# Kernel tuning notes

Measured on AMD Instinct MI355X. Metric: run time of the kernel, lower is better.

Reference implementation:

```python
import jax, jax.numpy as jnp
import numpy as np

N = 50000   # nodes
E = 300000  # edges
D = 256     # emb_dim
L = 5       # num_layers
BN_EPS = 1e-5


def setup_inputs() -> dict:
    key = jax.random.key(0)
    ks = jax.random.split(key, 6)
    scale = 0.05
    return {
        "x": jax.random.normal(ks[0], (N, D), jnp.float32),
        "src": jax.random.randint(ks[1], (E,), 0, N, dtype=jnp.int32),
        "dst": jax.random.randint(ks[2], (E,), 0, N, dtype=jnp.int32),
        "W1": jax.random.normal(ks[3], (L, D, D), jnp.float32) * scale,
        "b1": jnp.zeros((L, D), jnp.float32),
        "g1": jnp.ones((L, D), jnp.float32),
        "bt1": jnp.zeros((L, D), jnp.float32),
        "W2": jax.random.normal(ks[4], (L, D, D), jnp.float32) * scale,
        "b2": jnp.zeros((L, D), jnp.float32),
        "eps": jnp.zeros((L,), jnp.float32),
        "bn_g": jnp.ones((L, D), jnp.float32),
        "bn_b": jnp.zeros((L, D), jnp.float32),
    }


def _bn(h, gamma, beta):
    # torch BatchNorm1d training-mode forward: biased batch stats over nodes
    mean = jnp.mean(h, axis=0)
    var = jnp.var(h, axis=0)
    return (h - mean) * jax.lax.rsqrt(var + BN_EPS) * gamma + beta


def reference(x, src, dst, W1, b1, g1, bt1, W2, b2, eps, bn_g, bn_b):
    h = x
    for l in range(L):
        # GINConv: gather relu(x[src]) -> scatter-sum to dst
        msg = jax.nn.relu(h[src])                          # [E, D]
        agg = jax.ops.segment_sum(msg, dst, num_segments=N)  # [N, D]
        z = (1.0 + eps[l]) * h + agg
        # mlp: Linear -> BN -> ReLU -> Linear
        z = z @ W1[l] + b1[l]
        z = jax.nn.relu(_bn(z, g1[l], bt1[l]))
        z = z @ W2[l] + b2[l]
        # per-layer BatchNorm; dropout is identity (eval / drop_ratio=0)
        z = _bn(z, bn_g[l], bn_b[l])
        if l < L - 1:
            z = jax.nn.relu(z)
        h = z
    return h  # JK='last'
```

## Files before the change

kernel.cpp:

```cpp
#include <hip/hip_runtime.h>
#include <hip/hip_bf16.h>

#define N_NODES 50000
#define N_EDGES 300000
#define DIM 256
#define MPAD 50048

typedef __attribute__((ext_vector_type(8))) _Float16 half8;
typedef __attribute__((ext_vector_type(4))) _Float16 half4;
typedef __attribute__((ext_vector_type(4))) float f32x4;

__device__ __forceinline__ void async16(const void* g, void* l) {
    __builtin_amdgcn_global_load_lds(
        (const __attribute__((address_space(1))) unsigned int*)g,
        (__attribute__((address_space(3))) unsigned int*)l, 16, 0, 0);
}

__global__ __launch_bounds__(256) void hist_dst(const int* __restrict__ dst,
                                                int* __restrict__ deg, int E) {
    int e = blockIdx.x * blockDim.x + threadIdx.x;
    if (e < E) atomicAdd(&deg[dst[e]], 1);
}

__global__ __launch_bounds__(1024) void scan_blk(const int* __restrict__ deg,
                                                 int* __restrict__ ptr,
                                                 int* __restrict__ bsum, int n) {
    __shared__ int wsum[16];
    __shared__ int wpre[16];
    int tid = threadIdx.x;
    int i = blockIdx.x * 1024 + tid;
    int v = (i < n) ? deg[i] : 0;
    int lane = tid & 63, w = tid >> 6;
    int s = v;
#pragma unroll
    for (int off = 1; off < 64; off <<= 1) {
        int t = __shfl_up(s, off, 64);
        if (lane >= off) s += t;
    }
    if (lane == 63) wsum[w] = s;
    __syncthreads();
    if (tid < 16) {
        int acc = 0;
        for (int j = 0; j < tid; j++) acc += wsum[j];
        wpre[tid] = acc;
    }
    __syncthreads();
    int incl = s + wpre[w];
    if (i < n) ptr[i] = incl - v;
    if (tid == 1023) bsum[blockIdx.x] = incl;
}

__global__ __launch_bounds__(1024) void scan_add(int* __restrict__ ptr,
                                                 const int* __restrict__ bsum,
                                                 int* __restrict__ cursor,
                                                 int n, int E) {
    __shared__ int soff;
    int tid = threadIdx.x;
    if (tid < 64) {
        int v = (tid < (int)blockIdx.x) ? bsum[tid] : 0;
#pragma unroll
        for (int off = 32; off > 0; off >>= 1) v += __shfl_down(v, off, 64);
        if (tid == 0) soff = v;
    }
    __syncthreads();
    int i = blockIdx.x * 1024 + tid;
    if (i < n) {
        int val = ptr[i] + soff;
        ptr[i] = val;
        cursor[i] = val;
    }
    if (i == n) ptr[n] = E;
}

__global__ __launch_bounds__(256) void scatter_src(const int* __restrict__ src,
                                                   const int* __restrict__ dst,
                                                   int* __restrict__ cursor,
                                                   int* __restrict__ srcbuf, int E) {
    int e = blockIdx.x * blockDim.x + threadIdx.x;
    if (e < E) {
        int pos = atomicAdd(&cursor[dst[e]], 1);
        srcbuf[pos] = src[e];
    }
}

__global__ __launch_bounds__(256) void prep(const float* __restrict__ W1,
                                            const float* __restrict__ W2,
                                            _Float16* __restrict__ Wt,
                                            const float* __restrict__ x,
                                            _Float16* __restrict__ hb) {
    __shared__ float tile[64][65];
    int tid = threadIdx.x;
    if (blockIdx.x < 160) {
        int mat = blockIdx.x >> 4;
        int t = blockIdx.x & 15;
        int tr = t >> 2, tc = t & 3;
        const float* W = (mat < 5) ? (W1 + (size_t)mat * 65536)
                                   : (W2 + (size_t)(mat - 5) * 65536);
        int c = tid & 63, r0 = tid >> 6;
#pragma unroll 4
        for (int i = 0; i < 16; i++) {
            int r = r0 + i * 4;
            tile[r][c] = W[(size_t)(tr * 64 + r) * 256 + tc * 64 + c];
        }
        __syncthreads();
        _Float16* o = Wt + (size_t)mat * 65536;
#pragma unroll 4
        for (int i = 0; i < 16; i++) {
            int r = r0 + i * 4;
            o[(size_t)(tc * 64 + r) * 256 + tr * 64 + c] = (_Float16)tile[c][r];
        }
    } else {
        size_t i = (size_t)(blockIdx.x - 160) * 256 + tid;
        float4 v = ((const float4*)x)[i];
        half4 o;
        o.x = (_Float16)v.x; o.y = (_Float16)v.y;
        o.z = (_Float16)v.z; o.w = (_Float16)v.w;
        ((half4*)hb)[i] = o;
    }
}

__global__ __launch_bounds__(256) void gather_h(const _Float16* __restrict__ h,
                                                const int* __restrict__ ptr,
                                                const int* __restrict__ srcbuf,
                                                _Float16* __restrict__ z,
                                                const float* __restrict__ eps) {
    int node = blockIdx.x * 4 + (threadIdx.x >> 6);
    if (node >= N_NODES) return;
    int lane = threadIdx.x & 63;
    int beg = ptr[node], end = ptr[node + 1];
    float s = 1.0f + eps[0];
    half4 hv = ((const half4*)(h + (size_t)node * DIM))[lane];
    float a0 = (float)hv.x * s, a1 = (float)hv.y * s;
    float a2 = (float)hv.z * s, a3 = (float)hv.w * s;
    int e = beg;
    for (; e + 4 <= end; e += 4) {
        int s0 = srcbuf[e], s1 = srcbuf[e + 1], s2 = srcbuf[e + 2], s3 = srcbuf[e + 3];
        half4 v0 = ((const half4*)(h + (size_t)s0 * DIM))[lane];
        half4 v1 = ((const half4*)(h + (size_t)s1 * DIM))[lane];
        half4 v2 = ((const half4*)(h + (size_t)s2 * DIM))[lane];
        half4 v3 = ((const half4*)(h + (size_t)s3 * DIM))[lane];
        a0 += fmaxf((float)v0.x, 0.f) + fmaxf((float)v1.x, 0.f)
            + fmaxf((float)v2.x, 0.f) + fmaxf((float)v3.x, 0.f);
        a1 += fmaxf((float)v0.y, 0.f) + fmaxf((float)v1.y, 0.f)
            + fmaxf((float)v2.y, 0.f) + fmaxf((float)v3.y, 0.f);
        a2 += fmaxf((float)v0.z, 0.f) + fmaxf((float)v1.z, 0.f)
            + fmaxf((float)v2.z, 0.f) + fmaxf((float)v3.z, 0.f);
        a3 += fmaxf((float)v0.w, 0.f) + fmaxf((float)v1.w, 0.f)
            + fmaxf((float)v2.w, 0.f) + fmaxf((float)v3.w, 0.f);
    }
    for (; e < end; e++) {
        half4 v = ((const half4*)(h + (size_t)srcbuf[e] * DIM))[lane];
        a0 += fmaxf((float)v.x, 0.f); a1 += fmaxf((float)v.y, 0.f);
        a2 += fmaxf((float)v.z, 0.f); a3 += fmaxf((float)v.w, 0.f);
    }
    half4 o;
    o.x = (_Float16)a0; o.y = (_Float16)a1;
    o.z = (_Float16)a2; o.w = (_Float16)a3;
    ((half4*)(z + (size_t)node * DIM))[lane] = o;
}

__global__ __launch_bounds__(256) void gather_bn(const _Float16* __restrict__ C,
                                                 const int* __restrict__ ptr,
                                                 const int* __restrict__ srcbuf,
                                                 _Float16* __restrict__ z,
                                                 const float* __restrict__ scsh,
                                                 const float* __restrict__ eps,
                                                 int l) {
    int node = blockIdx.x * 4 + (threadIdx.x >> 6);
    if (node >= N_NODES) return;
    int lane = threadIdx.x & 63;
    float4 sc = ((const float4*)scsh)[lane];
    float4 sh = ((const float4*)(scsh + DIM))[lane];
    int beg = ptr[node], end = ptr[node + 1];
    float s = 1.0f + eps[l];
    half4 hv = ((const half4*)(C + (size_t)node * DIM))[lane];
    float a0 = s * fmaxf((float)hv.x * sc.x + sh.x, 0.f);
    float a1 = s * fmaxf((float)hv.y * sc.y + sh.y, 0.f);
    float a2 = s * fmaxf((float)hv.z * sc.z + sh.z, 0.f);
    float a3 = s * fmaxf((float)hv.w * sc.w + sh.w, 0.f);
    int e = beg;
    for (; e + 4 <= end; e += 4) {
        int s0 = srcbuf[e], s1 = srcbuf[e + 1], s2 = srcbuf[e + 2], s3 = srcbuf[e + 3];
        half4 v0 = ((const half4*)(C + (size_t)s0 * DIM))[lane];
        half4 v1 = ((const half4*)(C + (size_t)s1 * DIM))[lane];
        half4 v2 = ((const half4*)(C + (size_t)s2 * DIM))[lane];
        half4 v3 = ((const half4*)(C + (size_t)s3 * DIM))[lane];
        a0 += fmaxf((float)v0.x * sc.x + sh.x, 0.f) + fmaxf((float)v1.x * sc.x + sh.x, 0.f)
            + fmaxf((float)v2.x * sc.x + sh.x, 0.f) + fmaxf((float)v3.x * sc.x + sh.x, 0.f);
        a1 += fmaxf((float)v0.y * sc.y + sh.y, 0.f) + fmaxf((float)v1.y * sc.y + sh.y, 0.f)
            + fmaxf((float)v2.y * sc.y + sh.y, 0.f) + fmaxf((float)v3.y * sc.y + sh.y, 0.f);
        a2 += fmaxf((float)v0.z * sc.z + sh.z, 0.f) + fmaxf((float)v1.z * sc.z + sh.z, 0.f)
            + fmaxf((float)v2.z * sc.z + sh.z, 0.f) + fmaxf((float)v3.z * sc.z + sh.z, 0.f);
        a3 += fmaxf((float)v0.w * sc.w + sh.w, 0.f) + fmaxf((float)v1.w * sc.w + sh.w, 0.f)
            + fmaxf((float)v2.w * sc.w + sh.w, 0.f) + fmaxf((float)v3.w * sc.w + sh.w, 0.f);
    }
    for (; e < end; e++) {
        half4 v = ((const half4*)(C + (size_t)srcbuf[e] * DIM))[lane];
        a0 += fmaxf((float)v.x * sc.x + sh.x, 0.f);
        a1 += fmaxf((float)v.y * sc.y + sh.y, 0.f);
        a2 += fmaxf((float)v.z * sc.z + sh.z, 0.f);
        a3 += fmaxf((float)v.w * sc.w + sh.w, 0.f);
    }
    half4 o;
    o.x = (_Float16)a0; o.y = (_Float16)a1;
    o.z = (_Float16)a2; o.w = (_Float16)a3;
    ((half4*)(z + (size_t)node * DIM))[lane] = o;
}

#define GEMM_EPILOGUE                                                        \
    __syncthreads();                                                         \
    float* colsum = (float*)((char*)smem + 34816);                           \
    float* colsq = colsum + 128;                                             \
    if (tid < 128) { colsum[tid] = 0.0f; colsq[tid] = 0.0f; }                \
    _Float16* Cs = (_Float16*)smem;                                          \
    float bcol[4];                                                           \
    _Pragma("unroll")                                                        \
    for (int j = 0; j < 4; j++) bcol[j] = bias[col0 + wn + j * 16 + lrow];   \
    float csum[4] = {0.f, 0.f, 0.f, 0.f};                                    \
    float csq[4] = {0.f, 0.f, 0.f, 0.f};                                     \
    _Pragma("unroll")                                                        \
    for (int i = 0; i < 4; i++) {                                            \
        int rl = wm + i * 16 + quad * 4;                                     \
        _Pragma("unroll")                                                    \
        for (int j = 0; j < 4; j++) {                                        \
            int cl = wn + j * 16 + lrow;                                     \
            _Pragma("unroll")                                                \
            for (int r = 0; r < 4; r++) {                                    \
                float v = acc[i][j][r] + bcol[j];                            \
                Cs[(rl + r) * 136 + cl] = (_Float16)v;                       \
                if (row0 + rl + r < M) { csum[j] += v; csq[j] += v * v; }    \
            }                                                                \
        }                                                                    \
    }                                                                        \
    __syncthreads();                                                         \
    {                                                                        \
        int rgrp = lane >> 4, ch = lane & 15;                                \
        _Pragma("unroll")                                                    \
        for (int it = 0; it < 8; it++) {                                     \
            int row = wid * 32 + it * 4 + rgrp;                              \
            uint4 vv = *(const uint4*)(Cs + row * 136 + ch * 8);             \
            *(uint4*)(C + (size_t)(row0 + row) * DIM + col0 + ch * 8) = vv;  \
        }                                                                    \
    }                                                                        \
    _Pragma("unroll")                                                        \
    for (int j = 0; j < 4; j++) {                                            \
        atomicAdd(&colsum[wn + j * 16 + lrow], csum[j]);                     \
        atomicAdd(&colsq[wn + j * 16 + lrow], csq[j]);                       \
    }                                                                        \
    __syncthreads();                                                         \
    if (tid < 128) {                                                         \
        float* st = stats + (blockIdx.y & 7) * 512;                          \
        atomicAdd(&st[col0 + tid], colsum[tid]);                             \
        atomicAdd(&st[DIM + col0 + tid], colsq[tid]);                        \
    }

__global__ __launch_bounds__(256) void gemm_f16(const _Float16* __restrict__ A,
                                                const _Float16* __restrict__ Wt,
                                                const float* __restrict__ bias,
                                                _Float16* __restrict__ C,
                                                float* __restrict__ stats,
                                                int M) {
    __shared__ uint4 smem[2240];

    int tid = threadIdx.x;
    int wid = tid >> 6, lane = tid & 63;
    int quad = lane >> 4, lrow = lane & 15;
    int row0 = blockIdx.y * 128, col0 = blockIdx.x * 128;
    int wm = (wid & 1) * 64, wn = (wid >> 1) * 64;

    f32x4 acc[4][4] = {};
    const char* Ab = (const char*)A;
    const char* Bb = (const char*)Wt;

#pragma unroll
    for (int ko = 0; ko < 4; ko++) {
        int kb0 = ko * 128;
#pragma unroll
        for (int j = 0; j < 4; j++) {
            int sbase = wid * 256 + j * 64;
            int s = sbase + lane;
            int m = s >> 3;
            int c = (s & 7) ^ (m & 7);
            size_t go = (size_t)(row0 + m) * 512 + kb0 + c * 16;
            async16(Ab + go, (char*)smem + sbase * 16);
            size_t gob = (size_t)(col0 + m) * 512 + kb0 + c * 16;
            async16(Bb + gob, (char*)smem + 16384 + sbase * 16);
        }
        __syncthreads();
#pragma unroll
        for (int kc = 0; kc < 2; kc++) {
            half8 af[4], bf[4];
#pragma unroll
            for (int t = 0; t < 4; t++) {
                int ma = wm + t * 16 + lrow;
                int ca = kc * 4 + quad;
                af[t] = *(const half8*)((const char*)smem +
                                        (ma * 8 + (ca ^ (ma & 7))) * 16);
                int mb = wn + t * 16 + lrow;
                bf[t] = *(const half8*)((const char*)smem + 16384 +
                                        (mb * 8 + (ca ^ (mb & 7))) * 16);
            }
#pragma unroll
            for (int i = 0; i < 4; i++)
#pragma unroll
                for (int j2 = 0; j2 < 4; j2++)
                    acc[i][j2] = __builtin_amdgcn_mfma_f32_16x16x32_f16(
                        af[i], bf[j2], acc[i][j2], 0, 0, 0);
        }
        if (ko < 3) __syncthreads();
    }

    GEMM_EPILOGUE
}

__global__ __launch_bounds__(256) void gemm_bn(const _Float16* __restrict__ A,
                                               const _Float16* __restrict__ Wt,
                                               const float* __restrict__ bias,
                                               const float* __restrict__ scsh,
                                               _Float16* __restrict__ C,
                                               float* __restrict__ stats,
                                               int M) {
    __shared__ uint4 smem[2240];

    int tid = threadIdx.x;
    int wid = tid >> 6, lane = tid & 63;
    int quad = lane >> 4, lrow = lane & 15;
    int row0 = blockIdx.y * 128, col0 = blockIdx.x * 128;
    int wm = (wid & 1) * 64, wn = (wid >> 1) * 64;

    half8 scv[8], shv[8];
#pragma unroll
    for (int cc = 0; cc < 8; cc++) {
        int kk = cc * 32 + quad * 8;
        float4 s0 = *(const float4*)(scsh + kk);
        float4 s1 = *(const float4*)(scsh + kk + 4);
        float4 h0 = *(const float4*)(scsh + DIM + kk);
        float4 h1 = *(const float4*)(scsh + DIM + kk + 4);
        half8 sv = {(_Float16)s0.x, (_Float16)s0.y, (_Float16)s0.z, (_Float16)s0.w,
                    (_Float16)s1.x, (_Float16)s1.y, (_Float16)s1.z, (_Float16)s1.w};
        half8 hv = {(_Float16)h0.x, (_Float16)h0.y, (_Float16)h0.z, (_Float16)h0.w,
                    (_Float16)h1.x, (_Float16)h1.y, (_Float16)h1.z, (_Float16)h1.w};
        scv[cc] = sv;
        shv[cc] = hv;
    }

    f32x4 acc[4][4] = {};
    const char* Ab = (const char*)A;
    const char* Bb = (const char*)Wt;
    const half8 zerov = {0, 0, 0, 0, 0, 0, 0, 0};

#pragma unroll
    for (int ko = 0; ko < 4; ko++) {
        int kb0 = ko * 128;
#pragma unroll
        for (int j = 0; j < 4; j++) {
            int sbase = wid * 256 + j * 64;
            int s = sbase + lane;
            int m = s >> 3;
            int c = (s & 7) ^ (m & 7);
            size_t go = (size_t)(row0 + m) * 512 + kb0 + c * 16;
            async16(Ab + go, (char*)smem + sbase * 16);
            size_t gob = (size_t)(col0 + m) * 512 + kb0 + c * 16;
            async16(Bb + gob, (char*)smem + 16384 + sbase * 16);
        }
        __syncthreads();
#pragma unroll
        for (int kc = 0; kc < 2; kc++) {
            half8 af[4], bf[4];
            half8 sv = scv[ko * 2 + kc];
            half8 hv = shv[ko * 2 + kc];
#pragma unroll
            for (int t = 0; t < 4; t++) {
                int ma = wm + t * 16 + lrow;
                int ca = kc * 4 + quad;
                half8 a = *(const half8*)((const char*)smem +
                                          (ma * 8 + (ca ^ (ma & 7))) * 16);
                af[t] = __builtin_elementwise_max(a * sv + hv, zerov);
                int mb = wn + t * 16 + lrow;
                bf[t] = *(const half8*)((const char*)smem + 16384 +
                                        (mb * 8 + (ca ^ (mb & 7))) * 16);
            }
#pragma unroll
            for (int i = 0; i < 4; i++)
#pragma unroll
                for (int j2 = 0; j2 < 4; j2++)
                    acc[i][j2] = __builtin_amdgcn_mfma_f32_16x16x32_f16(
                        af[i], bf[j2], acc[i][j2], 0, 0, 0);
        }
        if (ko < 3) __syncthreads();
    }

    GEMM_EPILOGUE
}

__global__ __launch_bounds__(256) void bn_finalize(float* __restrict__ stats,
                                                   const float* __restrict__ g,
                                                   const float* __restrict__ beta,
                                                   float* __restrict__ scsh,
                                                   int n) {
    int d = threadIdx.x;
    float s = 0.0f, sq = 0.0f;
#pragma unroll
    for (int r = 0; r < 8; r++) {
        s += stats[r * 512 + d];
        sq += stats[r * 512 + 256 + d];
        stats[r * 512 + d] = 0.0f;
        stats[r * 512 + 256 + d] = 0.0f;
    }
    float invn = 1.0f / (float)n;
    float mean = s * invn;
    float var = sq * invn - mean * mean;
    float inv = rsqrtf(var + 1e-5f);
    float scale = g[d] * inv;
    scsh[d] = scale;
    scsh[DIM + d] = beta[d] - mean * scale;
}

__global__ __launch_bounds__(256) void bn_apply_f(const _Float16* __restrict__ in,
                                                  float* __restrict__ outf,
                                                  const float* __restrict__ scsh) {
    size_t i = (size_t)blockIdx.x * 256 + threadIdx.x;
    int c4 = (int)(i & 63);
    float4 sc = ((const float4*)scsh)[c4];
    float4 sh = ((const float4*)(scsh + DIM))[c4];
    half4 v = ((const half4*)in)[i];
    float4 o;
    o.x = (float)v.x * sc.x + sh.x;
    o.y = (float)v.y * sc.y + sh.y;
    o.z = (float)v.z * sc.z + sh.z;
    o.w = (float)v.w * sc.w + sh.w;
    ((float4*)outf)[i] = o;
}

extern "C" void kernel_launch(void* const* d_in, const int* in_sizes, int n_in,
                              void* d_out, int out_size, void* d_ws, size_t ws_size,
                              hipStream_t stream) {
    (void)in_sizes; (void)n_in; (void)out_size; (void)ws_size;
    const float* x   = (const float*)d_in[0];
    const int*   src = (const int*)d_in[1];
    const int*   dst = (const int*)d_in[2];
    const float* W1  = (const float*)d_in[3];
    const float* b1  = (const float*)d_in[4];
    const float* g1  = (const float*)d_in[5];
    const float* bt1 = (const float*)d_in[6];
    const float* W2  = (const float*)d_in[7];
    const float* b2  = (const float*)d_in[8];
    const float* eps = (const float*)d_in[9];
    const float* bng = (const float*)d_in[10];
    const float* bnb = (const float*)d_in[11];
    float* out = (float*)d_out;

    const int N = N_NODES, E = N_EDGES, D = DIM;
    size_t NDp = (size_t)MPAD * D;

    _Float16* gin  = (_Float16*)d_ws;
    _Float16* C1   = gin + NDp;
    _Float16* C2   = C1 + NDp;
    _Float16* Wt   = C2 + NDp;
    float* statsA  = (float*)(Wt + 10 * 65536);
    float* statsB  = statsA + 4096;
    int* deg       = (int*)(statsB + 4096);
    int* ptr       = deg + N;
    int* bsum      = ptr + N + 1;
    int* srcbuf    = bsum + 64;
    float* scshA   = (float*)(srcbuf + E);
    float* scshB   = scshA + 512;

    const int ELEM4_BLOCKS = N * D / 4 / 256;
    const int NODE_BLOCKS  = (N + 3) / 4;
    const int E_BLOCKS     = (E + 255) / 256;
    const int SCAN_BLOCKS  = (N + 1023) / 1024;
    const dim3 GEMM_GRID(2, MPAD / 128);

    hipMemsetAsync(statsA, 0, (size_t)(8192 + N) * sizeof(float), stream);
    hist_dst<<<E_BLOCKS, 256, 0, stream>>>(dst, deg, E);
    scan_blk<<<SCAN_BLOCKS, 1024, 0, stream>>>(deg, ptr, bsum, N);
    scan_add<<<SCAN_BLOCKS, 1024, 0, stream>>>(ptr, bsum, deg, N, E);
    scatter_src<<<E_BLOCKS, 256, 0, stream>>>(src, dst, deg, srcbuf, E);
    prep<<<160 + ELEM4_BLOCKS, 256, 0, stream>>>(W1, W2, Wt, x, C1);

    for (int l = 0; l < 5; l++) {
        if (l == 0)
            gather_h<<<NODE_BLOCKS, 256, 0, stream>>>(C1, ptr, srcbuf, gin, eps);
        else
            gather_bn<<<NODE_BLOCKS, 256, 0, stream>>>(C2, ptr, srcbuf, gin,
                                                       scshB, eps, l);

        gemm_f16<<<GEMM_GRID, 256, 0, stream>>>(
            gin, Wt + (size_t)l * 65536, b1 + (size_t)l * D, C1, statsA, N);
        bn_finalize<<<1, 256, 0, stream>>>(statsA, g1 + (size_t)l * D,
                                           bt1 + (size_t)l * D, scshA, N);

        gemm_bn<<<GEMM_GRID, 256, 0, stream>>>(
            C1, Wt + (size_t)(5 + l) * 65536, b2 + (size_t)l * D, scshA,
            C2, statsB, N);
        bn_finalize<<<1, 256, 0, stream>>>(statsB, bng + (size_t)l * D,
                                           bnb + (size_t)l * D, scshB, N);

        if (l == 4)
            bn_apply_f<<<ELEM4_BLOCKS, 256, 0, stream>>>(C2, out, scshB);
    }
}
```

Before: 628.3 us.

## Fold first BN finalize into second GEMM and rotate K order per block

The separate bn_finalize launch after the first GEMM is removed; each gemm_bn block now reduces the per-column statistics itself into shared memory before building its scale/shift vectors. Stats buffers become per-layer and are zeroed once up front, so the finalize kernels no longer need to clear them. Both GEMMs also rotate the starting K chunk by block row, which spreads concurrent blocks across different regions of the weight and activation data. The cost is redundant finalize work in every GEMM block, a little more shared memory, and a larger initial memset.

```diff
diff --git a/kernel.cpp b/kernel.cpp
--- a/kernel.cpp
+++ b/kernel.cpp
@@ -14,6 +14,25 @@
     __builtin_amdgcn_global_load_lds(
         (const __attribute__((address_space(1))) unsigned int*)g,
         (__attribute__((address_space(3))) unsigned int*)l, 16, 0, 0);
+}
+
+__device__ __forceinline__ void bn_finalize_thread(const float* __restrict__ st,
+                                                   const float* __restrict__ g,
+                                                   const float* __restrict__ beta,
+                                                   float* scshL, int d, int n) {
+    float s = 0.0f, sq = 0.0f;
+#pragma unroll
+    for (int r = 0; r < 8; r++) {
+        s += st[r * 512 + d];
+        sq += st[r * 512 + 256 + d];
+    }
+    float invn = 1.0f / (float)n;
+    float mean = s * invn;
+    float var = sq * invn - mean * mean;
+    float inv = rsqrtf(var + 1e-5f);
+    float scale = g[d] * inv;
+    scshL[d] = scale;
+    scshL[256 + d] = beta[d] - mean * scale;
 }
 
 __global__ __launch_bounds__(256) void hist_dst(const int* __restrict__ dst,
@@ -267,6 +286,7 @@
     int quad = lane >> 4, lrow = lane & 15;
     int row0 = blockIdx.y * 128, col0 = blockIdx.x * 128;
     int wm = (wid & 1) * 64, wn = (wid >> 1) * 64;
+    int krot = blockIdx.y & 3;
 
     f32x4 acc[4][4] = {};
     const char* Ab = (const char*)A;
@@ -274,7 +294,8 @@
 
 #pragma unroll
     for (int ko = 0; ko < 4; ko++) {
-        int kb0 = ko * 128;
+        int kr = (ko + krot) & 3;
+        int kb0 = kr * 128;
 #pragma unroll
         for (int j = 0; j < 4; j++) {
             int sbase = wid * 256 + j * 64;
@@ -316,26 +337,33 @@
 __global__ __launch_bounds__(256) void gemm_bn(const _Float16* __restrict__ A,
                                                const _Float16* __restrict__ Wt,
                                                const float* __restrict__ bias,
-                                               const float* __restrict__ scsh,
                                                _Float16* __restrict__ C,
                                                float* __restrict__ stats,
+                                               const float* __restrict__ statsIn,
+                                               const float* __restrict__ gamma1,
+                                               const float* __restrict__ beta1,
                                                int M) {
-    __shared__ uint4 smem[2240];
+    __shared__ uint4 smem[2368];
 
     int tid = threadIdx.x;
     int wid = tid >> 6, lane = tid & 63;
     int quad = lane >> 4, lrow = lane & 15;
     int row0 = blockIdx.y * 128, col0 = blockIdx.x * 128;
     int wm = (wid & 1) * 64, wn = (wid >> 1) * 64;
+    int krot = blockIdx.y & 3;
+
+    float* scshL = (float*)((char*)smem + 35840);
+    bn_finalize_thread(statsIn, gamma1, beta1, scshL, tid, M);
+    __syncthreads();
 
     half8 scv[8], shv[8];
 #pragma unroll
     for (int cc = 0; cc < 8; cc++) {
         int kk = cc * 32 + quad * 8;
-        float4 s0 = *(const float4*)(scsh + kk);
-        float4 s1 = *(const float4*)(scsh + kk + 4);
-        float4 h0 = *(const float4*)(scsh + DIM + kk);
-        float4 h1 = *(const float4*)(scsh + DIM + kk + 4);
+        float4 s0 = *(const float4*)(scshL + kk);
+        float4 s1 = *(const float4*)(scshL + kk + 4);
+        float4 h0 = *(const float4*)(scshL + DIM + kk);
+        float4 h1 = *(const float4*)(scshL + DIM + kk + 4);
         half8 sv = {(_Float16)s0.x, (_Float16)s0.y, (_Float16)s0.z, (_Float16)s0.w,
                     (_Float16)s1.x, (_Float16)s1.y, (_Float16)s1.z, (_Float16)s1.w};
         half8 hv = {(_Float16)h0.x, (_Float16)h0.y, (_Float16)h0.z, (_Float16)h0.w,
@@ -351,7 +379,8 @@
 
 #pragma unroll
     for (int ko = 0; ko < 4; ko++) {
-        int kb0 = ko * 128;
+        int kr = (ko + krot) & 3;
+        int kb0 = kr * 128;
 #pragma unroll
         for (int j = 0; j < 4; j++) {
             int sbase = wid * 256 + j * 64;
@@ -367,8 +396,8 @@
 #pragma unroll
         for (int kc = 0; kc < 2; kc++) {
             half8 af[4], bf[4];
-            half8 sv = scv[ko * 2 + kc];
-            half8 hv = shv[ko * 2 + kc];
+            half8 sv = scv[kr * 2 + kc];
+            half8 hv = shv[kr * 2 + kc];
 #pragma unroll
             for (int t = 0; t < 4; t++) {
                 int ma = wm + t * 16 + lrow;
@@ -393,7 +422,7 @@
     GEMM_EPILOGUE
 }
 
-__global__ __launch_bounds__(256) void bn_finalize(float* __restrict__ stats,
+__global__ __launch_bounds__(256) void bn_finalize(const float* __restrict__ stats,
                                                    const float* __restrict__ g,
                                                    const float* __restrict__ beta,
                                                    float* __restrict__ scsh,
@@ -404,8 +433,6 @@
     for (int r = 0; r < 8; r++) {
         s += stats[r * 512 + d];
         sq += stats[r * 512 + 256 + d];
-        stats[r * 512 + d] = 0.0f;
-        stats[r * 512 + 256 + d] = 0.0f;
     }
     float invn = 1.0f / (float)n;
     float mean = s * invn;
@@ -458,13 +485,12 @@
     _Float16* C2   = C1 + NDp;
     _Float16* Wt   = C2 + NDp;
     float* statsA  = (float*)(Wt + 10 * 65536);
-    float* statsB  = statsA + 4096;
-    int* deg       = (int*)(statsB + 4096);
+    float* statsB  = statsA + 5 * 4096;
+    int* deg       = (int*)(statsB + 5 * 4096);
     int* ptr       = deg + N;
     int* bsum      = ptr + N + 1;
     int* srcbuf    = bsum + 64;
-    float* scshA   = (float*)(srcbuf + E);
-    float* scshB   = scshA + 512;
+    float* scshB   = (float*)(srcbuf + E);
 
     const int ELEM4_BLOCKS = N * D / 4 / 256;
     const int NODE_BLOCKS  = (N + 3) / 4;
@@ -472,7 +498,7 @@
     const int SCAN_BLOCKS  = (N + 1023) / 1024;
     const dim3 GEMM_GRID(2, MPAD / 128);
 
-    hipMemsetAsync(statsA, 0, (size_t)(8192 + N) * sizeof(float), stream);
+    hipMemsetAsync(statsA, 0, (size_t)(10 * 4096 + N) * sizeof(float), stream);
     hist_dst<<<E_BLOCKS, 256, 0, stream>>>(dst, deg, E);
     scan_blk<<<SCAN_BLOCKS, 1024, 0, stream>>>(deg, ptr, bsum, N);
     scan_add<<<SCAN_BLOCKS, 1024, 0, stream>>>(ptr, bsum, deg, N, E);
@@ -480,6 +506,9 @@
     prep<<<160 + ELEM4_BLOCKS, 256, 0, stream>>>(W1, W2, Wt, x, C1);
 
     for (int l = 0; l < 5; l++) {
+        float* stA = statsA + (size_t)l * 4096;
+        float* stB = statsB + (size_t)l * 4096;
+
         if (l == 0)
             gather_h<<<NODE_BLOCKS, 256, 0, stream>>>(C1, ptr, srcbuf, gin, eps);
         else
@@ -487,14 +516,13 @@
                                                        scshB, eps, l);
 
         gemm_f16<<<GEMM_GRID, 256, 0, stream>>>(
-            gin, Wt + (size_t)l * 65536, b1 + (size_t)l * D, C1, statsA, N);
-        bn_finalize<<<1, 256, 0, stream>>>(statsA, g1 + (size_t)l * D,
-                                           bt1 + (size_t)l * D, scshA, N);
+            gin, Wt + (size_t)l * 65536, b1 + (size_t)l * D, C1, stA, N);
 
         gemm_bn<<<GEMM_GRID, 256, 0, stream>>>(
-            C1, Wt + (size_t)(5 + l) * 65536, b2 + (size_t)l * D, scshA,
-            C2, statsB, N);
-        bn_finalize<<<1, 256, 0, stream>>>(statsB, bng + (size_t)l * D,
+            C1, Wt + (size_t)(5 + l) * 65536, b2 + (size_t)l * D, C2,
+            stB, stA, g1 + (size_t)l * D, bt1 + (size_t)l * D, N);
+
+        bn_finalize<<<1, 256, 0, stream>>>(stB, bng + (size_t)l * D,
                                            bnb + (size_t)l * D, scshB, N);
 
         if (l == 4)
```

Result: slower. 1.334 ms (+112.3%).
